# Optimization experiments

Measured on AMD Instinct MI355X. Metric: run time of the kernel, lower is better.

The kernel has to match this reference:

```python
import jax, jax.numpy as jnp
import numpy as np

B, S, DIM = 32, 2048, 384
QK = DIM // 8          # 48
EXP = 2 * DIM          # 768, expand_factor = 2
NUM_BLOCKS = 8         # round(8*log2(1+1.0))
EPS = 1e-5


def setup_inputs() -> dict:
    key = jax.random.key(0)
    k1, k2, k3 = jax.random.split(key, 3)
    x = jax.random.normal(k1, (B, S, DIM), dtype=jnp.float32)
    norm_w = jnp.ones((DIM,), dtype=jnp.float32)  # LayerNorm weight, bias=False
    expand_w = (0.5 / DIM**0.5 / 2.0) * jax.random.normal(k2, (2 * QK + 2 * EXP, DIM), dtype=jnp.float32)
    project_w = (1.0 / DIM**0.5 / 2.0 / NUM_BLOCKS) * jax.random.normal(k3, (DIM, EXP), dtype=jnp.float32)
    pos_mult = jnp.array(1.0, dtype=jnp.float32)
    return {"x": x, "norm_w": norm_w, "expand_w": expand_w, "project_w": project_w, "pos_mult": pos_mult}


def reference(x, norm_w, expand_w, project_w, pos_mult):
    s = x.shape[1]
    residual = x
    # LayerNorm (no bias)
    mu = jnp.mean(x, axis=-1, keepdims=True)
    var = jnp.var(x, axis=-1, keepdims=True)
    xn = (x - mu) * jax.lax.rsqrt(var + EPS) * norm_w
    # fused expand projection -> query, key, linear, pre_gelu
    h = jnp.einsum('bsd,ed->bse', xn, expand_w)  # [B,S,2*QK+2*EXP]
    q = h[..., :QK]
    k = h[..., QK:2 * QK]
    lin = h[..., 2 * QK:2 * QK + EXP]
    pre = h[..., 2 * QK + EXP:]
    geglu = lin * jax.nn.gelu(pre, approximate=False)  # torch F.gelu default = erf
    geglu_local = geglu[..., :EXP - DIM]          # [B,S,EXP-DIM]
    geglu_value = geglu[..., EXP - DIM:]          # [B,S,DIM]
    # ALiBi-like additive causal mask
    idx = jnp.arange(s)
    pbb = (idx[None, :] - idx[:, None]).astype(x.dtype)       # [S,S], j - i (<=0 on allowed past)
    future = idx[None, :] > idx[:, None]                       # triu(diagonal=1)
    attn_mask = jnp.where(future, -jnp.inf, jax.nn.softplus(pos_mult) * pbb)
    # scaled dot product attention (single head, d_qk = QK)
    scores = jnp.einsum('bqd,bkd->bqk', q, k) / jnp.sqrt(jnp.array(QK, dtype=x.dtype))
    probs = jax.nn.softmax(scores + attn_mask[None], axis=-1)
    attention = jnp.einsum('bqk,bkd->bqd', probs, geglu_value)
    out = jnp.einsum('bse,de->bsd', jnp.concatenate([geglu_local, attention], axis=-1), project_w)
    return residual + out
```

## Files before the change

kernel.cpp:

```cpp
#include <hip/hip_runtime.h>
#include <hip/hip_bf16.h>
#include <math.h>

#define S_LEN 2048
#define NBATCH 32
#define DIM 384
#define NTOK (NBATCH * S_LEN)

typedef __hip_bfloat16 bf16;
typedef __attribute__((ext_vector_type(8))) short short8v;
typedef __attribute__((ext_vector_type(4))) float f32x4;
typedef __attribute__((ext_vector_type(2))) unsigned int uint2v;
typedef __attribute__((ext_vector_type(4))) int int4v;
typedef short8v fragT;

#define LDAP 72

__device__ __forceinline__ float bf2f(unsigned short u) {
  union { unsigned int i; float f; } c; c.i = ((unsigned int)u) << 16; return c.f;
}

__global__ __launch_bounds__(256) void conv_kernel(const float* __restrict__ we,
                                                   const float* __restrict__ wp,
                                                   bf16* __restrict__ web,
                                                   bf16* __restrict__ wpb) {
  int i = blockIdx.x * 256 + threadIdx.x;
  int stride = gridDim.x * 256;
  for (int j = i; j < 1632 * 384; j += stride) web[j] = __float2bfloat16(we[j]);
  for (int j = i; j < 384 * 768; j += stride) wpb[j] = __float2bfloat16(wp[j]);
}

__global__ __launch_bounds__(256) void ln_kernel(const float* __restrict__ x,
                                                 const float* __restrict__ nw,
                                                 bf16* __restrict__ xn) {
  int token = blockIdx.x * 4 + (threadIdx.x >> 6);
  int lane = threadIdx.x & 63;
  const float* xr = x + (size_t)token * DIM;
  float v[6];
  float s = 0.f, sq = 0.f;
#pragma unroll
  for (int j = 0; j < 6; ++j) {
    v[j] = xr[lane + j * 64];
    s += v[j];
    sq += v[j] * v[j];
  }
#pragma unroll
  for (int o = 32; o; o >>= 1) {
    s += __shfl_xor(s, o);
    sq += __shfl_xor(sq, o);
  }
  float mu = s * (1.f / DIM);
  float var = sq * (1.f / DIM) - mu * mu;
  float rs = rsqrtf(var + 1e-5f);
  bf16* xo = xn + (size_t)token * DIM;
#pragma unroll
  for (int j = 0; j < 6; ++j) {
    int c = lane + j * 64;
    xo[c] = __float2bfloat16((v[j] - mu) * rs * nw[c]);
  }
}

#define EBP 40
__global__ __launch_bounds__(256, 2) void expand_db_kernel(
    const bf16* __restrict__ xn, const bf16* __restrict__ web,
    bf16* __restrict__ qkb, bf16* __restrict__ gl, bf16* __restrict__ gv) {
  __shared__ short Abuf[2][128 * EBP];
  __shared__ short Bbuf[2][256 * EBP];
  int t = threadIdx.x;
  int lane = t & 63, w = t >> 6;
  int wr = w >> 1, wc = w & 1;
  int m = lane & 15, g = lane >> 4;

  int bid = blockIdx.x;
  int logical = (bid & 7) * 448 + (bid >> 3);
  int xt = logical / 7, y = logical % 7;
  int row0 = xt * 128;

  int aR[2], aS[2], bR[4], bS[4], bRow[4];
#pragma unroll
  for (int i = 0; i < 2; ++i) { int idx = i * 256 + t; aR[i] = idx >> 2; aS[i] = idx & 3; }
#pragma unroll
  for (int i = 0; i < 4; ++i) {
    int idx = i * 256 + t;
    bR[i] = idx >> 2; bS[i] = idx & 3;
    int r = bR[i], brow;
    if (y == 0) brow = (r < 96) ? r : 95;
    else {
      int c0 = (y - 1) * 128, half = r >> 7, nn = r & 127;
      brow = (nn < 64) ? (96 + c0 + half * 64 + nn) : (864 + c0 + half * 64 + (nn - 64));
    }
    bRow[i] = brow;
  }

  auto loadA = [&](int kt, short8v* d) {
#pragma unroll
    for (int i = 0; i < 2; ++i)
      d[i] = *reinterpret_cast<const short8v*>(xn + (size_t)(row0 + aR[i]) * 384 + kt * 32 + aS[i] * 8);
  };
  auto loadB = [&](int kt, short8v* d) {
#pragma unroll
    for (int i = 0; i < 4; ++i)
      d[i] = *reinterpret_cast<const short8v*>(web + (size_t)bRow[i] * 384 + kt * 32 + bS[i] * 8);
  };
  auto writeAB = [&](int p, const short8v* a, const short8v* b) {
#pragma unroll
    for (int i = 0; i < 2; ++i)
      *reinterpret_cast<short8v*>(&Abuf[p][aR[i] * EBP + aS[i] * 8]) = a[i];
#pragma unroll
    for (int i = 0; i < 4; ++i)
      *reinterpret_cast<short8v*>(&Bbuf[p][bR[i] * EBP + bS[i] * 8]) = b[i];
  };

  f32x4 acc[4][8];
#pragma unroll
  for (int i = 0; i < 4; ++i)
#pragma unroll
    for (int j = 0; j < 8; ++j) acc[i][j] = (f32x4){0.f, 0.f, 0.f, 0.f};

  short8v a0[2], b0[4], a1[2], b1[4];
  loadA(0, a0); loadB(0, b0);
  loadA(1, a1); loadB(1, b1);
  writeAB(0, a0, b0);
  __syncthreads();

#pragma unroll
  for (int s = 0; s < 12; ++s) {
    int p = s & 1;
    if (s < 11) {
      if (s & 1) writeAB(p ^ 1, a0, b0);
      else       writeAB(p ^ 1, a1, b1);
    }
    if (s < 10) {
      if (s & 1) { loadA(s + 2, a1); loadB(s + 2, b1); }
      else       { loadA(s + 2, a0); loadB(s + 2, b0); }
    }
    fragT af[4], bf8[8];
#pragma unroll
    for (int mi = 0; mi < 4; ++mi)
      af[mi] = *reinterpret_cast<const fragT*>(&Abuf[p][(wr * 64 + mi * 16 + m) * EBP + g * 8]);
#pragma unroll
    for (int ni = 0; ni < 8; ++ni)
      bf8[ni] = *reinterpret_cast<const fragT*>(&Bbuf[p][(wc * 128 + ni * 16 + m) * EBP + g * 8]);
    __builtin_amdgcn_s_setprio(1);
#pragma unroll
    for (int mi = 0; mi < 4; ++mi)
#pragma unroll
      for (int ni = 0; ni < 8; ++ni)
        acc[mi][ni] = __builtin_amdgcn_mfma_f32_16x16x32_bf16(af[mi], bf8[ni], acc[mi][ni], 0, 0, 0);
    __builtin_amdgcn_s_setprio(0);
    __syncthreads();
  }

  int cl = m, rg = g;
  if (y == 0) {
    if (wc == 0) {
#pragma unroll
      for (int mi = 0; mi < 4; ++mi)
#pragma unroll
        for (int ni = 0; ni < 6; ++ni) {
          int n = ni * 16 + cl;
          if (n < 96) {
#pragma unroll
            for (int r = 0; r < 4; ++r) {
              int token = row0 + wr * 64 + mi * 16 + rg * 4 + r;
              qkb[(size_t)token * 96 + n] = __float2bfloat16(acc[mi][ni][r]);
            }
          }
        }
    }
  } else {
    int c0 = (y - 1) * 128;
#pragma unroll
    for (int mi = 0; mi < 4; ++mi)
#pragma unroll
      for (int ni = 0; ni < 4; ++ni) {
        int c = c0 + wc * 64 + ni * 16 + cl;
#pragma unroll
        for (int r = 0; r < 4; ++r) {
          int token = row0 + wr * 64 + mi * 16 + rg * 4 + r;
          float lin = acc[mi][ni][r];
          float pre = acc[mi][ni + 4][r];
          float z = 0.79788456f * (pre + 0.044715f * pre * pre * pre);
          float gelu = pre * (1.f / (1.f + __expf(-2.f * z)));
          float gval = lin * gelu;
          if (c < 384)
            gl[(size_t)token * DIM + c] = __float2bfloat16(gval);
          else
            gv[(size_t)token * DIM + (c - 384)] = __float2bfloat16(gval);
        }
      }
  }
}

#define ATT_P_OFF 0
#define ATT_Q_OFF 8704
#define ATT_K_OFF 13312
#define ATT_S_OFF 31744
#define ATT_V0_OFF 8704
#define ATT_V1_OFF 36352
#define ATT_SMEM 64000

__global__ __launch_bounds__(256) void attn_mfma_kernel(
    const bf16* __restrict__ qkb, const bf16* __restrict__ gv,
    const float* __restrict__ pos_mult, bf16* __restrict__ ao) {
  __shared__ char smem[ATT_SMEM];
  bf16* P = (bf16*)(smem + ATT_P_OFF);
  bf16* Qs = (bf16*)(smem + ATT_Q_OFF);
  bf16* Ks = (bf16*)(smem + ATT_K_OFF);
  float* Ss = (float*)(smem + ATT_S_OFF);

  int t = threadIdx.x;
  int lane = t & 63;
  int w = t >> 6;
  int batch = blockIdx.x >> 6;
  int q0 = (blockIdx.x & 63) * 32;
  size_t tb = (size_t)batch * S_LEN;
  int jbase = q0 - 96;
  float cmul = log1pf(expf(pos_mult[0]));
  const float rs = 0.14433756729740643f;
  const short8v z8 = (short8v){0, 0, 0, 0, 0, 0, 0, 0};

  {
    int r = t >> 3, c = t & 7;
    short8v v = z8;
    if (c < 6) v = *reinterpret_cast<const short8v*>(qkb + (tb + q0 + r) * 96 + c * 8);
    *reinterpret_cast<short8v*>(Qs + r * LDAP + c * 8) = v;
  }
  {
    int r = t >> 1, h = t & 1;
    int j = jbase + r;
    if (j >= 0) {
      const bf16* krow = qkb + (tb + j) * 96 + 48 + h * 24;
      *reinterpret_cast<short8v*>(Ks + r * LDAP + h * 24) = *reinterpret_cast<const short8v*>(krow);
      *reinterpret_cast<short8v*>(Ks + r * LDAP + h * 24 + 8) = *reinterpret_cast<const short8v*>(krow + 8);
      *reinterpret_cast<short8v*>(Ks + r * LDAP + h * 24 + 16) = *reinterpret_cast<const short8v*>(krow + 16);
    } else {
      *reinterpret_cast<short8v*>(Ks + r * LDAP + h * 24) = z8;
      *reinterpret_cast<short8v*>(Ks + r * LDAP + h * 24 + 8) = z8;
      *reinterpret_cast<short8v*>(Ks + r * LDAP + h * 24 + 16) = z8;
    }
    if (h == 1) {
      *reinterpret_cast<short8v*>(Ks + r * LDAP + 48) = z8;
      *reinterpret_cast<short8v*>(Ks + r * LDAP + 56) = z8;
    }
  }
  __syncthreads();

  int m = lane & 15, g = lane >> 4;

  {
    f32x4 sacc[2][2];
#pragma unroll
    for (int mi = 0; mi < 2; ++mi)
#pragma unroll
      for (int ni = 0; ni < 2; ++ni) sacc[mi][ni] = (f32x4){0.f, 0.f, 0.f, 0.f};
#pragma unroll
    for (int ks = 0; ks < 2; ++ks) {
      int ko = ks * 32 + g * 8;
      fragT aq[2], bk[2];
#pragma unroll
      for (int mi = 0; mi < 2; ++mi)
        aq[mi] = *reinterpret_cast<const fragT*>(Qs + (mi * 16 + m) * LDAP + ko);
#pragma unroll
      for (int ni = 0; ni < 2; ++ni)
        bk[ni] = *reinterpret_cast<const fragT*>(Ks + (w * 32 + ni * 16 + m) * LDAP + ko);
#pragma unroll
      for (int mi = 0; mi < 2; ++mi)
#pragma unroll
        for (int ni = 0; ni < 2; ++ni)
          sacc[mi][ni] = __builtin_amdgcn_mfma_f32_16x16x32_bf16(aq[mi], bk[ni], sacc[mi][ni], 0, 0, 0);
    }
#pragma unroll
    for (int mi = 0; mi < 2; ++mi)
#pragma unroll
      for (int ni = 0; ni < 2; ++ni)
#pragma unroll
        for (int r = 0; r < 4; ++r) {
          int q = mi * 16 + g * 4 + r;
          int key = w * 32 + ni * 16 + m;
          int gi = q0 + q, gj = jbase + key;
          float s = (gj >= 0 && gj <= gi)
                        ? sacc[mi][ni][r] * rs + cmul * (float)(gj - gi)
                        : -INFINITY;
          Ss[q * 132 + key] = s;
        }
  }
  __syncthreads();

  auto stageV = [&](int c, unsigned bufoff) {
    int j = t >> 3;
    int c8 = t & 7;
    int gj = jbase + c * 32 + j;
    bf16* vb = (bf16*)(smem + bufoff);
    const bf16* vrow = gv + (tb + gj) * (size_t)DIM;
#pragma unroll
    for (int it = 0; it < 6; ++it) {
      int dj = c8 + it * 8;
      int d = dj * 8;
      short8v v = z8;
      if (gj >= 0) v = *reinterpret_cast<const short8v*>(vrow + d);
      *reinterpret_cast<short8v*>(vb + ((j >> 2) * 24 + (d >> 4)) * LDAP + (j & 3) * 16 + (d & 15)) = v;
    }
  };

  {
    int sq = t >> 3, sl = t & 7;
    union { float4 f4[4]; float f[16]; } su;
#pragma unroll
    for (int u = 0; u < 4; ++u)
      su.f4[u] = *reinterpret_cast<const float4*>(Ss + sq * 132 + sl * 16 + u * 4);
    __syncthreads();
    float mx = -INFINITY;
#pragma unroll
    for (int e = 0; e < 16; ++e) mx = fmaxf(mx, su.f[e]);
    mx = fmaxf(mx, __shfl_xor(mx, 1));
    mx = fmaxf(mx, __shfl_xor(mx, 2));
    mx = fmaxf(mx, __shfl_xor(mx, 4));
    float pv[16];
    float sum = 0.f;
#pragma unroll
    for (int e = 0; e < 16; ++e) {
      pv[e] = expf(su.f[e] - mx);
      sum += pv[e];
    }
    sum += __shfl_xor(sum, 1);
    sum += __shfl_xor(sum, 2);
    sum += __shfl_xor(sum, 4);
    float inv = 1.f / sum;
    union { bf16 b[16]; short8v s[2]; } pk;
#pragma unroll
    for (int e = 0; e < 16; ++e) pk.b[e] = __float2bfloat16(pv[e] * inv);
    bf16* pr = P + sq * 136 + sl * 16;
    *reinterpret_cast<short8v*>(pr) = pk.s[0];
    *reinterpret_cast<short8v*>(pr + 8) = pk.s[1];
  }
  stageV(0, ATT_V0_OFF);
  __syncthreads();

  f32x4 oacc[2][6];
#pragma unroll
  for (int mi = 0; mi < 2; ++mi)
#pragma unroll
    for (int nt = 0; nt < 6; ++nt) oacc[mi][nt] = (f32x4){0.f, 0.f, 0.f, 0.f};

  unsigned sbase = (unsigned)(size_t)(&smem[0]);
  unsigned lanebase = (unsigned)(((48 * g + 6 * w) * LDAP + m) * 2);

  for (int c = 0; c < 4; ++c) {
    unsigned vaddr = sbase + ((c & 1) ? ATT_V1_OFF : ATT_V0_OFF) + lanebase;
    fragT pa0 = *reinterpret_cast<const fragT*>(P + m * 136 + c * 32 + g * 8);
    fragT pa1 = *reinterpret_cast<const fragT*>(P + (16 + m) * 136 + c * 32 + g * 8);
    uint2v trr[12];
#pragma unroll
    for (int nt = 0; nt < 6; ++nt) {
      asm volatile("ds_read_b64_tr_b16 %0, %1" : "=v"(trr[2 * nt]) : "v"(vaddr + nt * 144));
      asm volatile("ds_read_b64_tr_b16 %0, %1" : "=v"(trr[2 * nt + 1]) : "v"(vaddr + nt * 144 + 3456));
    }
    asm volatile("s_waitcnt lgkmcnt(0)" ::: "memory");
    __builtin_amdgcn_sched_barrier(0);
    if (c < 3) stageV(c + 1, (c & 1) ? ATT_V0_OFF : ATT_V1_OFF);
#pragma unroll
    for (int nt = 0; nt < 6; ++nt) {
      union { int4v i4; fragT f; } u;
      u.i4 = (int4v){(int)trr[2 * nt].x, (int)trr[2 * nt].y,
                     (int)trr[2 * nt + 1].x, (int)trr[2 * nt + 1].y};
      oacc[0][nt] = __builtin_amdgcn_mfma_f32_16x16x32_bf16(pa0, u.f, oacc[0][nt], 0, 0, 0);
      oacc[1][nt] = __builtin_amdgcn_mfma_f32_16x16x32_bf16(pa1, u.f, oacc[1][nt], 0, 0, 0);
    }
    __syncthreads();
  }

#pragma unroll
  for (int mi = 0; mi < 2; ++mi)
#pragma unroll
    for (int nt = 0; nt < 6; ++nt) {
#pragma unroll
      for (int r = 0; r < 4; ++r) {
        int q = mi * 16 + g * 4 + r;
        int d = w * 96 + nt * 16 + m;
        ao[(tb + q0 + q) * (size_t)DIM + d] = __float2bfloat16(oacc[mi][nt][r]);
      }
    }
}

__global__ __launch_bounds__(256, 2) void project_db_kernel(
    const bf16* __restrict__ gl, const bf16* __restrict__ at,
    const bf16* __restrict__ wpb, const float* __restrict__ x,
    float* __restrict__ out) {
  __shared__ short Abuf[2][128 * LDAP];
  __shared__ short Bbuf[2][128 * LDAP];
  int t = threadIdx.x;
  int bid = blockIdx.x;
  int logical = (bid & 7) * 192 + (bid >> 3);
  int row0 = (logical / 3) * 128;
  int col0 = (logical % 3) * 128;
  int lane = t & 63, w = t >> 6;
  int wr = w >> 1, wc = w & 1;
  int m = lane & 15, g = lane >> 4;

  int rI[4], c8 = t & 7;
#pragma unroll
  for (int i = 0; i < 4; ++i) rI[i] = i * 32 + (t >> 3);

  auto loadA = [&](int kt, short8v* d) {
    const bf16* ab = (kt < 6) ? gl : at;
    int kk0 = (kt < 6 ? kt : kt - 6) * 64 + c8 * 8;
#pragma unroll
    for (int i = 0; i < 4; ++i)
      d[i] = *reinterpret_cast<const short8v*>(ab + (size_t)(row0 + rI[i]) * DIM + kk0);
  };
  auto loadB = [&](int kt, short8v* d) {
    int kk0 = kt * 64 + c8 * 8;
#pragma unroll
    for (int i = 0; i < 4; ++i)
      d[i] = *reinterpret_cast<const short8v*>(wpb + (size_t)(col0 + rI[i]) * 768 + kk0);
  };
  auto writeAB = [&](int p, const short8v* a, const short8v* b) {
#pragma unroll
    for (int i = 0; i < 4; ++i)
      *reinterpret_cast<short8v*>(&Abuf[p][rI[i] * LDAP + c8 * 8]) = a[i];
#pragma unroll
    for (int i = 0; i < 4; ++i)
      *reinterpret_cast<short8v*>(&Bbuf[p][rI[i] * LDAP + c8 * 8]) = b[i];
  };

  f32x4 acc[4][4];
#pragma unroll
  for (int i = 0; i < 4; ++i)
#pragma unroll
    for (int j = 0; j < 4; ++j) acc[i][j] = (f32x4){0.f, 0.f, 0.f, 0.f};

  short8v a0[4], b0[4], a1[4], b1[4];
  loadA(0, a0); loadB(0, b0);
  loadA(1, a1); loadB(1, b1);
  writeAB(0, a0, b0);
  __syncthreads();

#pragma unroll
  for (int s = 0; s < 12; ++s) {
    int p = s & 1;
    if (s < 11) {
      if (s & 1) writeAB(p ^ 1, a0, b0);
      else       writeAB(p ^ 1, a1, b1);
    }
    if (s < 10) {
      if (s & 1) { loadA(s + 2, a1); loadB(s + 2, b1); }
      else       { loadA(s + 2, a0); loadB(s + 2, b0); }
    }
#pragma unroll
    for (int ks = 0; ks < 2; ++ks) {
      int ko = ks * 32 + g * 8;
      fragT af[4], bfv[4];
#pragma unroll
      for (int mi = 0; mi < 4; ++mi)
        af[mi] = *reinterpret_cast<const fragT*>(&Abuf[p][(wr * 64 + mi * 16 + m) * LDAP + ko]);
#pragma unroll
      for (int ni = 0; ni < 4; ++ni)
        bfv[ni] = *reinterpret_cast<const fragT*>(&Bbuf[p][(wc * 64 + ni * 16 + m) * LDAP + ko]);
      __builtin_amdgcn_s_setprio(1);
#pragma unroll
      for (int mi = 0; mi < 4; ++mi)
#pragma unroll
        for (int ni = 0; ni < 4; ++ni)
          acc[mi][ni] = __builtin_amdgcn_mfma_f32_16x16x32_bf16(af[mi], bfv[ni], acc[mi][ni], 0, 0, 0);
      __builtin_amdgcn_s_setprio(0);
    }
    __syncthreads();
  }

#pragma unroll
  for (int mi = 0; mi < 4; ++mi)
#pragma unroll
    for (int ni = 0; ni < 4; ++ni) {
      int d = col0 + wc * 64 + ni * 16 + m;
#pragma unroll
      for (int r = 0; r < 4; ++r) {
        int token = row0 + wr * 64 + mi * 16 + g * 4 + r;
        out[(size_t)token * DIM + d] = x[(size_t)token * DIM + d] + acc[mi][ni][r];
      }
    }
}

extern "C" void kernel_launch(void* const* d_in, const int* in_sizes, int n_in,
                              void* d_out, int out_size, void* d_ws, size_t ws_size,
                              hipStream_t stream) {
  (void)in_sizes; (void)n_in; (void)out_size; (void)ws_size;
  const float* x = (const float*)d_in[0];
  const float* nw = (const float*)d_in[1];
  const float* we = (const float*)d_in[2];
  const float* wp = (const float*)d_in[3];
  const float* pm = (const float*)d_in[4];
  char* ws = (char*)d_ws;
  bf16* xn = (bf16*)(ws);
  bf16* qk = (bf16*)(ws + 50331648);
  bf16* gl = (bf16*)(ws + 62914560);
  bf16* gv = (bf16*)(ws + 113246208);
  bf16* at = (bf16*)(ws + 163577856);
  bf16* web = (bf16*)(ws + 163577856);
  bf16* wpb = (bf16*)(ws + 213909504);
  float* out = (float*)d_out;

  hipLaunchKernelGGL(conv_kernel, dim3(512), dim3(256), 0, stream, we, wp, web, wpb);
  hipLaunchKernelGGL(ln_kernel, dim3(NTOK / 4), dim3(256), 0, stream, x, nw, xn);
  hipLaunchKernelGGL(expand_db_kernel, dim3(512 * 7), dim3(256), 0, stream, xn, web, qk, gl, gv);
  hipLaunchKernelGGL(attn_mfma_kernel, dim3(NBATCH * (S_LEN / 32)), dim3(256), 0, stream, qk, gv, pm, at);
  hipLaunchKernelGGL(project_db_kernel, dim3(512 * 3), dim3(256), 0, stream, gl, at, wpb, x, out);
}
```

Measured before the change: 279.8 us.

## Load GEMM tiles directly into LDS with global_load_lds and XOR swizzle

```diff
diff --git a/kernel.cpp b/kernel.cpp
--- a/kernel.cpp
+++ b/kernel.cpp
@@ -18,6 +18,12 @@
 
 __device__ __forceinline__ float bf2f(unsigned short u) {
   union { unsigned int i; float f; } c; c.i = ((unsigned int)u) << 16; return c.f;
+}
+
+__device__ __forceinline__ void gl16(const bf16* g, short* l) {
+  __builtin_amdgcn_global_load_lds(
+      (const __attribute__((address_space(1))) void*)g,
+      (__attribute__((address_space(3))) void*)l, 16, 0, 0);
 }
 
 __global__ __launch_bounds__(256) void conv_kernel(const float* __restrict__ we,
@@ -60,12 +66,11 @@
   }
 }
 
-#define EBP 40
-__global__ __launch_bounds__(256, 2) void expand_db_kernel(
+__global__ __launch_bounds__(256, 2) void expand_gl_kernel(
     const bf16* __restrict__ xn, const bf16* __restrict__ web,
     bf16* __restrict__ qkb, bf16* __restrict__ gl, bf16* __restrict__ gv) {
-  __shared__ short Abuf[2][128 * EBP];
-  __shared__ short Bbuf[2][256 * EBP];
+  __shared__ short As2[128 * 64];
+  __shared__ short Bs2[256 * 64];
   int t = threadIdx.x;
   int lane = t & 63, w = t >> 6;
   int wr = w >> 1, wc = w & 1;
@@ -76,40 +81,34 @@
   int xt = logical / 7, y = logical % 7;
   int row0 = xt * 128;
 
-  int aR[2], aS[2], bR[4], bS[4], bRow[4];
-#pragma unroll
-  for (int i = 0; i < 2; ++i) { int idx = i * 256 + t; aR[i] = idx >> 2; aS[i] = idx & 3; }
+  int lr = lane >> 3;
+  int s8 = lane & 7;
+  int cs = s8 ^ lr;
+
+  const bf16* ga[4];
+  const bf16* gb[8];
 #pragma unroll
   for (int i = 0; i < 4; ++i) {
-    int idx = i * 256 + t;
-    bR[i] = idx >> 2; bS[i] = idx & 3;
-    int r = bR[i], brow;
-    if (y == 0) brow = (r < 96) ? r : 95;
+    int row = w * 32 + i * 8 + lr;
+    ga[i] = xn + (size_t)(row0 + row) * 384 + cs * 8;
+  }
+#pragma unroll
+  for (int i = 0; i < 8; ++i) {
+    int row = w * 64 + i * 8 + lr;
+    int brow;
+    if (y == 0) brow = (row < 96) ? row : 95;
     else {
-      int c0 = (y - 1) * 128, half = r >> 7, nn = r & 127;
+      int c0 = (y - 1) * 128, half = row >> 7, nn = row & 127;
       brow = (nn < 64) ? (96 + c0 + half * 64 + nn) : (864 + c0 + half * 64 + (nn - 64));
     }
-    bRow[i] = brow;
-  }
-
-  auto loadA = [&](int kt, short8v* d) {
-#pragma unroll
-    for (int i = 0; i < 2; ++i)
-      d[i] = *reinterpret_cast<const short8v*>(xn + (size_t)(row0 + aR[i]) * 384 + kt * 32 + aS[i] * 8);
-  };
-  auto loadB = [&](int kt, short8v* d) {
-#pragma unroll
-    for (int i = 0; i < 4; ++i)
-      d[i] = *reinterpret_cast<const short8v*>(web + (size_t)bRow[i] * 384 + kt * 32 + bS[i] * 8);
-  };
-  auto writeAB = [&](int p, const short8v* a, const short8v* b) {
-#pragma unroll
-    for (int i = 0; i < 2; ++i)
-      *reinterpret_cast<short8v*>(&Abuf[p][aR[i] * EBP + aS[i] * 8]) = a[i];
-#pragma unroll
-    for (int i = 0; i < 4; ++i)
-      *reinterpret_cast<short8v*>(&Bbuf[p][bR[i] * EBP + bS[i] * 8]) = b[i];
-  };
+    gb[i] = web + (size_t)brow * 384 + cs * 8;
+  }
+  short* la[4];
+  short* lb[8];
+#pragma unroll
+  for (int i = 0; i < 4; ++i) la[i] = As2 + (w * 4 + i) * 512;
+#pragma unroll
+  for (int i = 0; i < 8; ++i) lb[i] = Bs2 + (w * 8 + i) * 512;
 
   f32x4 acc[4][8];
 #pragma unroll
@@ -117,38 +116,37 @@
 #pragma unroll
     for (int j = 0; j < 8; ++j) acc[i][j] = (f32x4){0.f, 0.f, 0.f, 0.f};
 
-  short8v a0[2], b0[4], a1[2], b1[4];
-  loadA(0, a0); loadB(0, b0);
-  loadA(1, a1); loadB(1, b1);
-  writeAB(0, a0, b0);
-  __syncthreads();
-
-#pragma unroll
-  for (int s = 0; s < 12; ++s) {
-    int p = s & 1;
-    if (s < 11) {
-      if (s & 1) writeAB(p ^ 1, a0, b0);
-      else       writeAB(p ^ 1, a1, b1);
-    }
-    if (s < 10) {
-      if (s & 1) { loadA(s + 2, a1); loadB(s + 2, b1); }
-      else       { loadA(s + 2, a0); loadB(s + 2, b0); }
-    }
-    fragT af[4], bf8[8];
-#pragma unroll
-    for (int mi = 0; mi < 4; ++mi)
-      af[mi] = *reinterpret_cast<const fragT*>(&Abuf[p][(wr * 64 + mi * 16 + m) * EBP + g * 8]);
-#pragma unroll
-    for (int ni = 0; ni < 8; ++ni)
-      bf8[ni] = *reinterpret_cast<const fragT*>(&Bbuf[p][(wc * 128 + ni * 16 + m) * EBP + g * 8]);
-    __builtin_amdgcn_s_setprio(1);
-#pragma unroll
-    for (int mi = 0; mi < 4; ++mi)
-#pragma unroll
-      for (int ni = 0; ni < 8; ++ni)
-        acc[mi][ni] = __builtin_amdgcn_mfma_f32_16x16x32_bf16(af[mi], bf8[ni], acc[mi][ni], 0, 0, 0);
-    __builtin_amdgcn_s_setprio(0);
-    __syncthreads();
+#pragma unroll
+  for (int kt = 0; kt < 6; ++kt) {
+    __syncthreads();
+#pragma unroll
+    for (int i = 0; i < 4; ++i) gl16(ga[i] + kt * 64, la[i]);
+#pragma unroll
+    for (int i = 0; i < 8; ++i) gl16(gb[i] + kt * 64, lb[i]);
+    __syncthreads();
+#pragma unroll
+    for (int ks = 0; ks < 2; ++ks) {
+      int c = ks * 4 + g;
+      int cxm = c ^ (m & 7);
+      fragT af[4], bf8[8];
+#pragma unroll
+      for (int mi = 0; mi < 4; ++mi) {
+        int R = wr * 64 + mi * 16 + m;
+        af[mi] = *reinterpret_cast<const fragT*>(&As2[R * 64 + cxm * 8]);
+      }
+#pragma unroll
+      for (int ni = 0; ni < 8; ++ni) {
+        int R = wc * 128 + ni * 16 + m;
+        bf8[ni] = *reinterpret_cast<const fragT*>(&Bs2[R * 64 + cxm * 8]);
+      }
+      __builtin_amdgcn_s_setprio(1);
+#pragma unroll
+      for (int mi = 0; mi < 4; ++mi)
+#pragma unroll
+        for (int ni = 0; ni < 8; ++ni)
+          acc[mi][ni] = __builtin_amdgcn_mfma_f32_16x16x32_bf16(af[mi], bf8[ni], acc[mi][ni], 0, 0, 0);
+      __builtin_amdgcn_s_setprio(0);
+    }
   }
 
   int cl = m, rg = g;
@@ -383,12 +381,12 @@
     }
 }
 
-__global__ __launch_bounds__(256, 2) void project_db_kernel(
+__global__ __launch_bounds__(256, 2) void project_gl_kernel(
     const bf16* __restrict__ gl, const bf16* __restrict__ at,
     const bf16* __restrict__ wpb, const float* __restrict__ x,
     float* __restrict__ out) {
-  __shared__ short Abuf[2][128 * LDAP];
-  __shared__ short Bbuf[2][128 * LDAP];
+  __shared__ short As2[128 * 64];
+  __shared__ short Bs2[128 * 64];
   int t = threadIdx.x;
   int bid = blockIdx.x;
   int logical = (bid & 7) * 192 + (bid >> 3);
@@ -398,65 +396,57 @@
   int wr = w >> 1, wc = w & 1;
   int m = lane & 15, g = lane >> 4;
 
-  int rI[4], c8 = t & 7;
-#pragma unroll
-  for (int i = 0; i < 4; ++i) rI[i] = i * 32 + (t >> 3);
-
-  auto loadA = [&](int kt, short8v* d) {
+  int lr = lane >> 3;
+  int s8 = lane & 7;
+  int cs = s8 ^ lr;
+
+  size_t aoff[4];
+  const bf16* gbp[4];
+#pragma unroll
+  for (int i = 0; i < 4; ++i) {
+    int row = w * 32 + i * 8 + lr;
+    aoff[i] = (size_t)(row0 + row) * 384 + cs * 8;
+    gbp[i] = wpb + (size_t)(col0 + row) * 768 + cs * 8;
+  }
+  short* la[4];
+  short* lb[4];
+#pragma unroll
+  for (int i = 0; i < 4; ++i) {
+    la[i] = As2 + (w * 4 + i) * 512;
+    lb[i] = Bs2 + (w * 4 + i) * 512;
+  }
+
+  f32x4 acc[4][4];
+#pragma unroll
+  for (int i = 0; i < 4; ++i)
+#pragma unroll
+    for (int j = 0; j < 4; ++j) acc[i][j] = (f32x4){0.f, 0.f, 0.f, 0.f};
+
+#pragma unroll
+  for (int kt = 0; kt < 12; ++kt) {
     const bf16* ab = (kt < 6) ? gl : at;
-    int kk0 = (kt < 6 ? kt : kt - 6) * 64 + c8 * 8;
-#pragma unroll
-    for (int i = 0; i < 4; ++i)
-      d[i] = *reinterpret_cast<const short8v*>(ab + (size_t)(row0 + rI[i]) * DIM + kk0);
-  };
-  auto loadB = [&](int kt, short8v* d) {
-    int kk0 = kt * 64 + c8 * 8;
-#pragma unroll
-    for (int i = 0; i < 4; ++i)
-      d[i] = *reinterpret_cast<const short8v*>(wpb + (size_t)(col0 + rI[i]) * 768 + kk0);
-  };
-  auto writeAB = [&](int p, const short8v* a, const short8v* b) {
-#pragma unroll
-    for (int i = 0; i < 4; ++i)
-      *reinterpret_cast<short8v*>(&Abuf[p][rI[i] * LDAP + c8 * 8]) = a[i];
-#pragma unroll
-    for (int i = 0; i < 4; ++i)
-      *reinterpret_cast<short8v*>(&Bbuf[p][rI[i] * LDAP + c8 * 8]) = b[i];
-  };
-
-  f32x4 acc[4][4];
-#pragma unroll
-  for (int i = 0; i < 4; ++i)
-#pragma unroll
-    for (int j = 0; j < 4; ++j) acc[i][j] = (f32x4){0.f, 0.f, 0.f, 0.f};
-
-  short8v a0[4], b0[4], a1[4], b1[4];
-  loadA(0, a0); loadB(0, b0);
-  loadA(1, a1); loadB(1, b1);
-  writeAB(0, a0, b0);
-  __syncthreads();
-
-#pragma unroll
-  for (int s = 0; s < 12; ++s) {
-    int p = s & 1;
-    if (s < 11) {
-      if (s & 1) writeAB(p ^ 1, a0, b0);
-      else       writeAB(p ^ 1, a1, b1);
-    }
-    if (s < 10) {
-      if (s & 1) { loadA(s + 2, a1); loadB(s + 2, b1); }
-      else       { loadA(s + 2, a0); loadB(s + 2, b0); }
-    }
+    int kk = (kt < 6 ? kt : kt - 6) * 64;
+    __syncthreads();
+#pragma unroll
+    for (int i = 0; i < 4; ++i) gl16(ab + aoff[i] + kk, la[i]);
+#pragma unroll
+    for (int i = 0; i < 4; ++i) gl16(gbp[i] + kt * 64, lb[i]);
+    __syncthreads();
 #pragma unroll
     for (int ks = 0; ks < 2; ++ks) {
-      int ko = ks * 32 + g * 8;
+      int c = ks * 4 + g;
+      int cxm = c ^ (m & 7);
       fragT af[4], bfv[4];
 #pragma unroll
-      for (int mi = 0; mi < 4; ++mi)
-        af[mi] = *reinterpret_cast<const fragT*>(&Abuf[p][(wr * 64 + mi * 16 + m) * LDAP + ko]);
-#pragma unroll
-      for (int ni = 0; ni < 4; ++ni)
-        bfv[ni] = *reinterpret_cast<const fragT*>(&Bbuf[p][(wc * 64 + ni * 16 + m) * LDAP + ko]);
+      for (int mi = 0; mi < 4; ++mi) {
+        int R = wr * 64 + mi * 16 + m;
+        af[mi] = *reinterpret_cast<const fragT*>(&As2[R * 64 + cxm * 8]);
+      }
+#pragma unroll
+      for (int ni = 0; ni < 4; ++ni) {
+        int R = wc * 64 + ni * 16 + m;
+        bfv[ni] = *reinterpret_cast<const fragT*>(&Bs2[R * 64 + cxm * 8]);
+      }
       __builtin_amdgcn_s_setprio(1);
 #pragma unroll
       for (int mi = 0; mi < 4; ++mi)
@@ -465,7 +455,6 @@
           acc[mi][ni] = __builtin_amdgcn_mfma_f32_16x16x32_bf16(af[mi], bfv[ni], acc[mi][ni], 0, 0, 0);
       __builtin_amdgcn_s_setprio(0);
     }
-    __syncthreads();
   }
 
 #pragma unroll
@@ -502,7 +491,7 @@
 
   hipLaunchKernelGGL(conv_kernel, dim3(512), dim3(256), 0, stream, we, wp, web, wpb);
   hipLaunchKernelGGL(ln_kernel, dim3(NTOK / 4), dim3(256), 0, stream, x, nw, xn);
-  hipLaunchKernelGGL(expand_db_kernel, dim3(512 * 7), dim3(256), 0, stream, xn, web, qk, gl, gv);
+  hipLaunchKernelGGL(expand_gl_kernel, dim3(512 * 7), dim3(256), 0, stream, xn, web, qk, gl, gv);
   hipLaunchKernelGGL(attn_mfma_kernel, dim3(NBATCH * (S_LEN / 32)), dim3(256), 0, stream, qk, gv, pm, at);
-  hipLaunchKernelGGL(project_db_kernel, dim3(512 * 3), dim3(256), 0, stream, gl, at, wpb, x, out);
-}
+  hipLaunchKernelGGL(project_gl_kernel, dim3(512 * 3), dim3(256), 0, stream, gl, at, wpb, x, out);
+}
```

Measured after the change: 266.9 us. 1.05x faster.
